# Kernel tuning notes

Hardware: AMD Instinct MI355X
Metric: run time of the kernel (lower is better)

## Reference

```python
import jax, jax.numpy as jnp
import numpy as np

K = 9  # knn kernel_size
SLOPE = 0.01  # LeakyReLU slope inside EdgeConv MLP (PyGraphBipartite default)


def setup_inputs() -> dict:
    key = jax.random.key(0)
    ks = jax.random.split(key, 5)
    B, C, H, W = 8, 96, 64, 64
    x = jax.random.normal(ks[0], (B, C, H, W), dtype=jnp.float32)
    # EdgeConv MLP: Linear(2C -> C), LeakyReLU(0.01), Linear(C -> C)
    W1 = jax.random.normal(ks[1], (2 * C, C), dtype=jnp.float32) * (1.0 / np.sqrt(2 * C))
    b1 = jax.random.normal(ks[2], (C,), dtype=jnp.float32) * 0.01
    W2 = jax.random.normal(ks[3], (C, C), dtype=jnp.float32) * (1.0 / np.sqrt(C))
    b2 = jax.random.normal(ks[4], (C,), dtype=jnp.float32) * 0.01
    return {"x": x, "W1": W1, "b1": b1, "W2": W2, "b2": b2}


def reference(x, W1, b1, W2, b2):
    B, C, H, W = x.shape
    M = H * W
    # flat_nodes: (B,C,H,W) -> per-image node features (B, M, C)
    xf = jnp.transpose(x, (0, 2, 3, 1)).reshape(B, M, C)

    # k-NN graph per image (batch-restricted), loop=True so self is a neighbor (dist 0)
    sq = jnp.sum(xf * xf, axis=-1)  # (B, M)
    dist = sq[:, :, None] + sq[:, None, :] - 2.0 * jnp.einsum("bmc,bnc->bmn", xf, xf)
    _, idx = jax.lax.top_k(-dist, K)  # (B, M, K) neighbor indices per center node

    # gather neighbor features: (B, M, K, C)
    xj = jax.vmap(lambda f, i: f[i])(xf, idx)
    xi = xf[:, :, None, :]  # center node, broadcast over K

    # EdgeConv message: MLP([x_i ; x_j - x_i]), then mean over neighbors
    feat = jnp.concatenate([jnp.broadcast_to(xi, xj.shape), xj - xi], axis=-1)  # (B,M,K,2C)
    h = feat @ W1 + b1
    h = jnp.where(h >= 0, h, SLOPE * h)  # LeakyReLU(0.01)
    h = h @ W2 + b2  # (B, M, K, C)
    out = jnp.mean(h, axis=2)  # mean aggregation -> (B, M, C)

    # norm='none' (Identity), act='relu'
    out = jax.nn.relu(out)

    # unflat_nodes: (B, M, C) -> (B, C, H, W)
    return jnp.transpose(out.reshape(B, H, W, C), (0, 3, 1, 2))
```

## Files before the change

kernel.cpp:

```cpp
#include <hip/hip_runtime.h>

#define B_ 8
#define C_ 96
#define CP_ 104
#define M_ 4096
#define K_ 9

typedef _Float16 f16x8 __attribute__((ext_vector_type(8)));
typedef float f32x4 __attribute__((ext_vector_type(4)));

typedef const __attribute__((address_space(1))) unsigned int* as1_u32p;
typedef __attribute__((address_space(3))) unsigned int* as3_u32p;

__device__ inline void g2lds16(const void* g, void* l) {
  __builtin_amdgcn_global_load_lds((as1_u32p)g, (as3_u32p)l, 16, 0, 0);
}

#define INSERT(dv, nv) do {                                                   \
    const int pz_ = tpos;                                                     \
    _Pragma("unroll")                                                         \
    for (int k_ = 0; k_ < K_; ++k_) if (k_ == pz_) { tv[k_] = (dv); ti[k_] = (nv); } \
    float mx_ = tv[0]; int mp_ = 0;                                           \
    _Pragma("unroll")                                                         \
    for (int k_ = 1; k_ < K_; ++k_) if (tv[k_] > mx_) { mx_ = tv[k_]; mp_ = k_; } \
    tmax = mx_; tpos = mp_;                                                   \
  } while (0)

__global__ __launch_bounds__(256) void prep1_kernel(
    const float* __restrict__ x, float* __restrict__ sq,
    unsigned short* __restrict__ xhi, unsigned short* __restrict__ xlo) {
  __shared__ float Xt[C_][64];
  const int b = blockIdx.y, m0 = blockIdx.x * 64, tid = threadIdx.x;
  const float* xb = x + (size_t)b * C_ * M_;
  for (int i = tid; i < C_ * 16; i += 256) {
    int c = i >> 4, j4 = (i & 15) << 2;
    *(float4*)&Xt[c][j4] = *(const float4*)&xb[(size_t)c * M_ + m0 + j4];
  }
  __syncthreads();
  if (tid < 64) {
    float s = 0.f;
#pragma unroll
    for (int c = 0; c < C_; ++c) { float v = Xt[c][tid]; s += v * v; }
    sq[b * M_ + m0 + tid] = s;
  }
  const int p = tid & 63, part = tid >> 6;
  union { unsigned short u[24]; uint4 q[3]; } hb, lb;
#pragma unroll
  for (int i = 0; i < 24; ++i) {
    float v = Xt[part * 24 + i][p];
    _Float16 h = (_Float16)v;
    _Float16 l = (_Float16)(v - (float)h);
    hb.u[i] = __builtin_bit_cast(unsigned short, h);
    lb.u[i] = __builtin_bit_cast(unsigned short, l);
  }
  size_t base = ((size_t)b * M_ + m0 + p) * CP_ + part * 24;
#pragma unroll
  for (int i = 0; i < 3; ++i) {
    *(uint4*)&xhi[base + i * 8] = hb.q[i];
    *(uint4*)&xlo[base + i * 8] = lb.q[i];
  }
}

__global__ __launch_bounds__(256, 3) void knn_kernel(
    const unsigned short* __restrict__ xhi, const unsigned short* __restrict__ xlo,
    const float* __restrict__ sq, int* __restrict__ idxw) {
  __shared__ struct { unsigned short bhi[64 * CP_]; unsigned short blo[64 * CP_]; } S[2];
  __shared__ float sqc[2][64];
  const int b = blockIdx.y, r0 = blockIdx.x * 64, tid = threadIdx.x;
  const int lane = tid & 63, w = tid >> 6;
  const int fp = lane & 15, kg = lane >> 4;
  const size_t bm = (size_t)b * M_;

  f16x8 qhi[3], qlo[3];
#pragma unroll
  for (int kt = 0; kt < 3; ++kt) {
    size_t off = (bm + r0 + w * 16 + fp) * CP_ + kt * 32 + kg * 8;
    qhi[kt] = *(const f16x8*)&xhi[off];
    qlo[kt] = *(const f16x8*)&xlo[off];
  }

  float tv[K_]; int ti[K_]; float tmax = 3.4e38f; int tpos = 0;
#pragma unroll
  for (int k = 0; k < K_; ++k) { tv[k] = 3.4e38f; ti[k] = 0; }

  auto stage = [&](int n0, int pp) {
    const unsigned short* sh = xhi + (bm + n0) * CP_;
    const unsigned short* sl = xlo + (bm + n0) * CP_;
    unsigned short* dh = S[pp].bhi;
    unsigned short* dl = S[pp].blo;
#pragma unroll
    for (int it = 0; it < 3; ++it) {
      int ch = tid + it * 256;
      g2lds16(sh + ch * 8, dh + ch * 8);
      g2lds16(sl + ch * 8, dl + ch * 8);
    }
    if (tid < 64) {
      int ch = 768 + tid;
      g2lds16(sh + ch * 8, dh + ch * 8);
      g2lds16(sl + ch * 8, dl + ch * 8);
      sqc[pp][tid] = sq[bm + n0 + tid];
    }
  };

  stage(0, 0);
  for (int t = 0; t < 64; ++t) {
    const int n0 = t * 64;
    const int cur = t & 1;
    __syncthreads();
    if (t < 63) stage(n0 + 64, cur ^ 1);

    float b0d = 0.f, b1d = 0.f; int b0n = 0, b1n = 0, bcnt = 0;

#pragma unroll
    for (int rs = 0; rs < 4; ++rs) {
      f16x8 nh[3], nl[3];
#pragma unroll
      for (int kt = 0; kt < 3; ++kt) {
        int boff = (rs * 16 + fp) * CP_ + kt * 32 + kg * 8;
        nh[kt] = *(const f16x8*)&S[cur].bhi[boff];
        nl[kt] = *(const f16x8*)&S[cur].blo[boff];
      }
      f32x4 acc = {0.f, 0.f, 0.f, 0.f};
#pragma unroll
      for (int kt = 0; kt < 3; ++kt) {
        acc = __builtin_amdgcn_mfma_f32_16x16x32_f16(nh[kt], qhi[kt], acc, 0, 0, 0);
        acc = __builtin_amdgcn_mfma_f32_16x16x32_f16(nh[kt], qlo[kt], acc, 0, 0, 0);
        acc = __builtin_amdgcn_mfma_f32_16x16x32_f16(nl[kt], qhi[kt], acc, 0, 0, 0);
      }
#pragma unroll
      for (int r = 0; r < 4; ++r) {
        const int nrow = rs * 16 + kg * 4 + r;
        const float d = sqc[cur][nrow] - 2.f * acc[r];
        if (d < tmax) {
          const int n = n0 + nrow;
          if (bcnt == 2) {
            if (b0d < tmax) INSERT(b0d, b0n);
            b0d = b1d; b0n = b1n;
            b1d = d;   b1n = n;
          } else if (bcnt == 1) {
            b1d = d; b1n = n; bcnt = 2;
          } else {
            b0d = d; b0n = n; bcnt = 1;
          }
        }
      }
    }
    if (bcnt >= 1 && b0d < tmax) INSERT(b0d, b0n);
    if (bcnt == 2 && b1d < tmax) INSERT(b1d, b1n);
  }

  __syncthreads();
  float* mv = (float*)&S[0];
  int*   mi = (int*)((char*)&S[0] + 64 * 37 * 4);
  const int qrow = w * 16 + fp;
#pragma unroll
  for (int k = 0; k < K_; ++k) {
    mv[qrow * 37 + kg * K_ + k] = tv[k];
    mi[qrow * 37 + kg * K_ + k] = ti[k];
  }
  __syncthreads();
  if (tid < 64) {
    float fv[K_]; int fi[K_];
    float mx = 3.4e38f; int mp = 0;
#pragma unroll
    for (int k = 0; k < K_; ++k) { fv[k] = 3.4e38f; fi[k] = 0; }
    for (int s = 0; s < 36; ++s) {
      float v = mv[tid * 37 + s]; int id = mi[tid * 37 + s];
      if (v < mx) {
#pragma unroll
        for (int k = 0; k < K_; ++k) if (k == mp) { fv[k] = v; fi[k] = id; }
        float m2 = fv[0]; int p2 = 0;
#pragma unroll
        for (int k = 1; k < K_; ++k) if (fv[k] > m2) { m2 = fv[k]; p2 = k; }
        mx = m2; mp = p2;
      }
    }
#pragma unroll
    for (int k = 0; k < K_; ++k)
      idxw[((size_t)b * M_ + r0 + tid) * K_ + k] = fi[k];
  }
}

__global__ __launch_bounds__(256) void prep2_kernel(
    const float* __restrict__ x, const float* __restrict__ W1,
    const float* __restrict__ b1, float* __restrict__ P, float* __restrict__ Q) {
  __shared__ float Xt[C_][64];
  __shared__ float Wt[C_][64];
  const int b = blockIdx.y, m0 = blockIdx.x * 64;
  const int tid = threadIdx.x;
  const float* xb = x + (size_t)b * C_ * M_;

  for (int i = tid; i < C_ * 16; i += 256) {
    int c = i >> 4, j4 = (i & 15) << 2;
    *(float4*)&Xt[c][j4] = *(const float4*)&xb[(size_t)c * M_ + m0 + j4];
  }

  const int ty = tid >> 4, tx = tid & 15;
  for (int t = 0; t < 3; ++t) {
    const int u0 = t * 64;
    __syncthreads();
    for (int i = tid; i < C_ * 64; i += 256) {
      int cin = i >> 6, j = i & 63;
      int u = u0 + j;
      float wv;
      if (u < C_) wv = W1[cin * C_ + u] - W1[(C_ + cin) * C_ + u];
      else        wv = W1[(C_ + cin) * C_ + (u - C_)];
      Wt[cin][j] = wv;
    }
    __syncthreads();
    float acc[4][4] = {};
#pragma unroll 8
    for (int c = 0; c < C_; ++c) {
      float4 rr = *(const float4*)&Xt[c][ty << 2];
      float4 ww = *(const float4*)&Wt[c][tx << 2];
      acc[0][0] += rr.x * ww.x; acc[0][1] += rr.x * ww.y; acc[0][2] += rr.x * ww.z; acc[0][3] += rr.x * ww.w;
      acc[1][0] += rr.y * ww.x; acc[1][1] += rr.y * ww.y; acc[1][2] += rr.y * ww.z; acc[1][3] += rr.y * ww.w;
      acc[2][0] += rr.z * ww.x; acc[2][1] += rr.z * ww.y; acc[2][2] += rr.z * ww.z; acc[2][3] += rr.z * ww.w;
      acc[3][0] += rr.w * ww.x; acc[3][1] += rr.w * ww.y; acc[3][2] += rr.w * ww.z; acc[3][3] += rr.w * ww.w;
    }
#pragma unroll
    for (int i = 0; i < 4; ++i) {
      int m = m0 + (ty << 2) + i;
      size_t base = ((size_t)b * M_ + m) * C_;
#pragma unroll
      for (int j = 0; j < 4; ++j) {
        int u = u0 + (tx << 2) + j;
        float v = acc[i][j];
        if (u < C_) P[base + u] = v + b1[u];
        else        Q[base + (u - C_)] = v;
      }
    }
  }
}

__global__ __launch_bounds__(256) void edge_mlp_kernel(
    const float* __restrict__ P, const float* __restrict__ Q,
    const int* __restrict__ idxw, const float* __restrict__ W2,
    const float* __restrict__ b2, float* __restrict__ out) {
  __shared__ float g_l[C_][64];
  __shared__ float W2t[C_ * C_];
  const int b = blockIdx.y, m0 = blockIdx.x * 64;
  const int tid = threadIdx.x;

  for (int i = tid; i < (C_ * C_) / 4; i += 256)
    *(float4*)&W2t[i * 4] = *(const float4*)&W2[i * 4];

  const int ml = tid & 63, cg = tid >> 6;
  const int m = m0 + ml;
  const float* prow = P + ((size_t)b * M_ + m) * C_ + cg * 24;
  float pr[24];
#pragma unroll
  for (int t = 0; t < 24; t += 4) {
    float4 v = *(const float4*)(prow + t);
    pr[t] = v.x; pr[t + 1] = v.y; pr[t + 2] = v.z; pr[t + 3] = v.w;
  }
  float gacc[24] = {};
  const int* irow = idxw + ((size_t)b * M_ + m) * K_;
#pragma unroll
  for (int k = 0; k < K_; ++k) {
    int j = irow[k];
    const float* qrow = Q + ((size_t)b * M_ + j) * C_ + cg * 24;
#pragma unroll
    for (int t = 0; t < 24; t += 4) {
      float4 qv = *(const float4*)(qrow + t);
      float h;
      h = pr[t + 0] + qv.x; gacc[t + 0] += (h >= 0.f) ? h : 0.01f * h;
      h = pr[t + 1] + qv.y; gacc[t + 1] += (h >= 0.f) ? h : 0.01f * h;
      h = pr[t + 2] + qv.z; gacc[t + 2] += (h >= 0.f) ? h : 0.01f * h;
      h = pr[t + 3] + qv.w; gacc[t + 3] += (h >= 0.f) ? h : 0.01f * h;
    }
  }
#pragma unroll
  for (int t = 0; t < 24; ++t) g_l[cg * 24 + t][ml] = gacc[t] * (1.f / 9.f);
  __syncthreads();

  const int ty = tid >> 4, tx = tid & 15;
  float acc2[4][6] = {};
#pragma unroll 4
  for (int c = 0; c < C_; ++c) {
    float4 rr = *(const float4*)&g_l[c][ty << 2];
    float2 wa = *(const float2*)&W2t[c * C_ + tx * 6];
    float2 wb = *(const float2*)&W2t[c * C_ + tx * 6 + 2];
    float2 wc = *(const float2*)&W2t[c * C_ + tx * 6 + 4];
    float rv[4] = {rr.x, rr.y, rr.z, rr.w};
    float wv[6] = {wa.x, wa.y, wb.x, wb.y, wc.x, wc.y};
#pragma unroll
    for (int i = 0; i < 4; ++i)
#pragma unroll
      for (int j = 0; j < 6; ++j) acc2[i][j] += rv[i] * wv[j];
  }
#pragma unroll
  for (int i = 0; i < 4; ++i) {
    int mm = m0 + (ty << 2) + i;
#pragma unroll
    for (int j = 0; j < 6; ++j) {
      int u = tx * 6 + j;
      float v = acc2[i][j] + b2[u];
      v = fmaxf(v, 0.f);
      out[((size_t)b * C_ + u) * M_ + mm] = v;
    }
  }
}

extern "C" void kernel_launch(void* const* d_in, const int* in_sizes, int n_in,
                              void* d_out, int out_size, void* d_ws, size_t ws_size,
                              hipStream_t stream) {
  const float* x  = (const float*)d_in[0];
  const float* W1 = (const float*)d_in[1];
  const float* b1 = (const float*)d_in[2];
  const float* W2 = (const float*)d_in[3];
  const float* b2 = (const float*)d_in[4];
  float* out = (float*)d_out;

  char* ws = (char*)d_ws;
  float* sq  = (float*)ws;
  int* idxw  = (int*)(ws + 131072);
  unsigned short* xhi = (unsigned short*)(ws + 1310720);
  unsigned short* xlo = (unsigned short*)(ws + 8126464);
  float* P = (float*)(ws + 1310720);
  float* Q = (float*)(ws + 13893632);

  dim3 grid(M_ / 64, B_), blk(256);
  prep1_kernel<<<grid, blk, 0, stream>>>(x, sq, xhi, xlo);
  knn_kernel<<<grid, blk, 0, stream>>>(xhi, xlo, sq, idxw);
  prep2_kernel<<<grid, blk, 0, stream>>>(x, W1, b1, P, Q);
  edge_mlp_kernel<<<grid, blk, 0, stream>>>(P, Q, idxw, W2, b2, out);
}
```

Before: 297.2 us.

## Split kNN candidate range across blocks, read neighbors directly from global, add merge kernel

The kNN kernel now splits each query tile's candidate range into two halves handled by separate blocks (grid z dimension), which doubles the number of blocks to improve occupancy and load balance. Each half writes its partial top-9 distances and indices to workspace, and a new merge kernel combines them. The LDS double-buffered staging through global_load_lds is removed in favour of direct per-lane global loads of neighbor fragments, relying on L2/L1 hits, and launch bounds are raised to 4 blocks per CU. Costs include an extra kernel launch, extra workspace traffic, and losing explicit LDS reuse of neighbor tiles across the four waves.

```diff
diff --git a/kernel.cpp b/kernel.cpp
--- a/kernel.cpp
+++ b/kernel.cpp
@@ -5,16 +5,11 @@
 #define CP_ 104
 #define M_ 4096
 #define K_ 9
+#define NSPLIT 2
+#define NHALF (M_ / NSPLIT)
 
 typedef _Float16 f16x8 __attribute__((ext_vector_type(8)));
 typedef float f32x4 __attribute__((ext_vector_type(4)));
-
-typedef const __attribute__((address_space(1))) unsigned int* as1_u32p;
-typedef __attribute__((address_space(3))) unsigned int* as3_u32p;
-
-__device__ inline void g2lds16(const void* g, void* l) {
-  __builtin_amdgcn_global_load_lds((as1_u32p)g, (as3_u32p)l, 16, 0, 0);
-}
 
 #define INSERT(dv, nv) do {                                                   \
     const int pz_ = tpos;                                                     \
@@ -61,15 +56,17 @@
   }
 }
 
-__global__ __launch_bounds__(256, 3) void knn_kernel(
+__global__ __launch_bounds__(256, 4) void knn_kernel(
     const unsigned short* __restrict__ xhi, const unsigned short* __restrict__ xlo,
-    const float* __restrict__ sq, int* __restrict__ idxw) {
-  __shared__ struct { unsigned short bhi[64 * CP_]; unsigned short blo[64 * CP_]; } S[2];
-  __shared__ float sqc[2][64];
-  const int b = blockIdx.y, r0 = blockIdx.x * 64, tid = threadIdx.x;
+    const float* __restrict__ sq, float* __restrict__ pv, int* __restrict__ pi) {
+  __shared__ float mv[64 * 37];
+  __shared__ int   mi[64 * 37];
+  const int b = blockIdx.y, r0 = blockIdx.x * 64, h = blockIdx.z;
+  const int tid = threadIdx.x;
   const int lane = tid & 63, w = tid >> 6;
   const int fp = lane & 15, kg = lane >> 4;
   const size_t bm = (size_t)b * M_;
+  const int nbeg = h * NHALF;
 
   f16x8 qhi[3], qlo[3];
 #pragma unroll
@@ -83,56 +80,38 @@
 #pragma unroll
   for (int k = 0; k < K_; ++k) { tv[k] = 3.4e38f; ti[k] = 0; }
 
-  auto stage = [&](int n0, int pp) {
-    const unsigned short* sh = xhi + (bm + n0) * CP_;
-    const unsigned short* sl = xlo + (bm + n0) * CP_;
-    unsigned short* dh = S[pp].bhi;
-    unsigned short* dl = S[pp].blo;
-#pragma unroll
-    for (int it = 0; it < 3; ++it) {
-      int ch = tid + it * 256;
-      g2lds16(sh + ch * 8, dh + ch * 8);
-      g2lds16(sl + ch * 8, dl + ch * 8);
-    }
-    if (tid < 64) {
-      int ch = 768 + tid;
-      g2lds16(sh + ch * 8, dh + ch * 8);
-      g2lds16(sl + ch * 8, dl + ch * 8);
-      sqc[pp][tid] = sq[bm + n0 + tid];
-    }
-  };
-
-  stage(0, 0);
-  for (int t = 0; t < 64; ++t) {
-    const int n0 = t * 64;
-    const int cur = t & 1;
-    __syncthreads();
-    if (t < 63) stage(n0 + 64, cur ^ 1);
-
+  const unsigned short* nbh = xhi + (bm + nbeg + fp) * CP_ + kg * 8;
+  const unsigned short* nbl = xlo + (bm + nbeg + fp) * CP_ + kg * 8;
+  const float* sqb = sq + bm + nbeg + kg * 4;
+
+  for (int t = 0; t < NHALF / 64; ++t) {
+    const int tb = t * 64;
     float b0d = 0.f, b1d = 0.f; int b0n = 0, b1n = 0, bcnt = 0;
-
 #pragma unroll
     for (int rs = 0; rs < 4; ++rs) {
-      f16x8 nh[3], nl[3];
-#pragma unroll
-      for (int kt = 0; kt < 3; ++kt) {
-        int boff = (rs * 16 + fp) * CP_ + kt * 32 + kg * 8;
-        nh[kt] = *(const f16x8*)&S[cur].bhi[boff];
-        nl[kt] = *(const f16x8*)&S[cur].blo[boff];
-      }
+      const size_t ro = (size_t)(tb + rs * 16) * CP_;
+      f16x8 nh0 = *(const f16x8*)(nbh + ro);
+      f16x8 nh1 = *(const f16x8*)(nbh + ro + 32);
+      f16x8 nh2 = *(const f16x8*)(nbh + ro + 64);
+      f16x8 nl0 = *(const f16x8*)(nbl + ro);
+      f16x8 nl1 = *(const f16x8*)(nbl + ro + 32);
+      f16x8 nl2 = *(const f16x8*)(nbl + ro + 64);
+      const f32x4 sqv = *(const f32x4*)&sqb[tb + rs * 16];
       f32x4 acc = {0.f, 0.f, 0.f, 0.f};
-#pragma unroll
-      for (int kt = 0; kt < 3; ++kt) {
-        acc = __builtin_amdgcn_mfma_f32_16x16x32_f16(nh[kt], qhi[kt], acc, 0, 0, 0);
-        acc = __builtin_amdgcn_mfma_f32_16x16x32_f16(nh[kt], qlo[kt], acc, 0, 0, 0);
-        acc = __builtin_amdgcn_mfma_f32_16x16x32_f16(nl[kt], qhi[kt], acc, 0, 0, 0);
-      }
+      acc = __builtin_amdgcn_mfma_f32_16x16x32_f16(nh0, qhi[0], acc, 0, 0, 0);
+      acc = __builtin_amdgcn_mfma_f32_16x16x32_f16(nh1, qhi[1], acc, 0, 0, 0);
+      acc = __builtin_amdgcn_mfma_f32_16x16x32_f16(nh2, qhi[2], acc, 0, 0, 0);
+      acc = __builtin_amdgcn_mfma_f32_16x16x32_f16(nh0, qlo[0], acc, 0, 0, 0);
+      acc = __builtin_amdgcn_mfma_f32_16x16x32_f16(nh1, qlo[1], acc, 0, 0, 0);
+      acc = __builtin_amdgcn_mfma_f32_16x16x32_f16(nh2, qlo[2], acc, 0, 0, 0);
+      acc = __builtin_amdgcn_mfma_f32_16x16x32_f16(nl0, qhi[0], acc, 0, 0, 0);
+      acc = __builtin_amdgcn_mfma_f32_16x16x32_f16(nl1, qhi[1], acc, 0, 0, 0);
+      acc = __builtin_amdgcn_mfma_f32_16x16x32_f16(nl2, qhi[2], acc, 0, 0, 0);
 #pragma unroll
       for (int r = 0; r < 4; ++r) {
-        const int nrow = rs * 16 + kg * 4 + r;
-        const float d = sqc[cur][nrow] - 2.f * acc[r];
+        const float d = sqv[r] - 2.f * acc[r];
         if (d < tmax) {
-          const int n = n0 + nrow;
+          const int n = nbeg + tb + rs * 16 + kg * 4 + r;
           if (bcnt == 2) {
             if (b0d < tmax) INSERT(b0d, b0n);
             b0d = b1d; b0n = b1n;
@@ -149,9 +128,6 @@
     if (bcnt == 2 && b1d < tmax) INSERT(b1d, b1n);
   }
 
-  __syncthreads();
-  float* mv = (float*)&S[0];
-  int*   mi = (int*)((char*)&S[0] + 64 * 37 * 4);
   const int qrow = w * 16 + fp;
 #pragma unroll
   for (int k = 0; k < K_; ++k) {
@@ -175,10 +151,35 @@
         mx = m2; mp = p2;
       }
     }
-#pragma unroll
-    for (int k = 0; k < K_; ++k)
-      idxw[((size_t)b * M_ + r0 + tid) * K_ + k] = fi[k];
-  }
+    size_t base = ((size_t)h * B_ * M_ + bm + r0 + tid) * K_;
+#pragma unroll
+    for (int k = 0; k < K_; ++k) { pv[base + k] = fv[k]; pi[base + k] = fi[k]; }
+  }
+}
+
+__global__ __launch_bounds__(256) void knn_merge_kernel(
+    const float* __restrict__ pv, const int* __restrict__ pi,
+    int* __restrict__ idxw) {
+  const int g = blockIdx.x * 256 + threadIdx.x;
+  float tv[K_]; int ti[K_]; float tmax = 3.4e38f; int tpos = 0;
+#pragma unroll
+  for (int k = 0; k < K_; ++k) { tv[k] = 3.4e38f; ti[k] = 0; }
+  const float* v0 = pv + (size_t)g * K_;
+  const int*   i0 = pi + (size_t)g * K_;
+  const float* v1 = pv + ((size_t)B_ * M_ + g) * K_;
+  const int*   i1 = pi + ((size_t)B_ * M_ + g) * K_;
+#pragma unroll
+  for (int s = 0; s < K_; ++s) {
+    float d = v0[s];
+    if (d < tmax) { int n = i0[s]; INSERT(d, n); }
+  }
+#pragma unroll
+  for (int s = 0; s < K_; ++s) {
+    float d = v1[s];
+    if (d < tmax) { int n = i1[s]; INSERT(d, n); }
+  }
+#pragma unroll
+  for (int k = 0; k < K_; ++k) idxw[(size_t)g * K_ + k] = ti[k];
 }
 
 __global__ __launch_bounds__(256) void prep2_kernel(
@@ -317,12 +318,15 @@
   int* idxw  = (int*)(ws + 131072);
   unsigned short* xhi = (unsigned short*)(ws + 1310720);
   unsigned short* xlo = (unsigned short*)(ws + 8126464);
+  float* pv = (float*)(ws + 14942208);
+  int*   pi = (int*)(ws + 17301504);
   float* P = (float*)(ws + 1310720);
   float* Q = (float*)(ws + 13893632);
 
-  dim3 grid(M_ / 64, B_), blk(256);
-  prep1_kernel<<<grid, blk, 0, stream>>>(x, sq, xhi, xlo);
-  knn_kernel<<<grid, blk, 0, stream>>>(xhi, xlo, sq, idxw);
-  prep2_kernel<<<grid, blk, 0, stream>>>(x, W1, b1, P, Q);
-  edge_mlp_kernel<<<grid, blk, 0, stream>>>(P, Q, idxw, W2, b2, out);
-}
+  dim3 blk(256);
+  prep1_kernel<<<dim3(M_ / 64, B_), blk, 0, stream>>>(x, sq, xhi, xlo);
+  knn_kernel<<<dim3(M_ / 64, B_, NSPLIT), blk, 0, stream>>>(xhi, xlo, sq, pv, pi);
+  knn_merge_kernel<<<dim3(B_ * M_ / 256), blk, 0, stream>>>(pv, pi, idxw);
+  prep2_kernel<<<dim3(M_ / 64, B_), blk, 0, stream>>>(x, W1, b1, P, Q);
+  edge_mlp_kernel<<<dim3(M_ / 64, B_), blk, 0, stream>>>(P, Q, idxw, W2, b2, out);
+}
```

Measured after the change: 313.1 us. +5.3%, slower.

## Split kNN candidate scan across blocks and merge partial top-k lists

Applied to the files above, without the earlier changes.

Adds a third grid dimension that splits each query tile's scan over candidate nodes into four independent chunks. Each chunk writes its partial top-9 distances and indices to workspace, and a new merge kernel combines them into the final index list. The aim is to raise block count and waves per CU so the MFMA-based distance scan hides latency better, at the cost of an extra launch and extra global traffic for the partial results. The two-entry candidate buffer is also now flushed only once after the tile loop, instead of after every tile.

```diff
diff --git a/kernel.cpp b/kernel.cpp
--- a/kernel.cpp
+++ b/kernel.cpp
@@ -5,6 +5,9 @@
 #define CP_ 104
 #define M_ 4096
 #define K_ 9
+#define NSPLIT 4
+#define NPART (M_ / NSPLIT)
+#define NTILES (NPART / 64)
 
 typedef _Float16 f16x8 __attribute__((ext_vector_type(8)));
 typedef float f32x4 __attribute__((ext_vector_type(4)));
@@ -63,13 +66,15 @@
 
 __global__ __launch_bounds__(256, 3) void knn_kernel(
     const unsigned short* __restrict__ xhi, const unsigned short* __restrict__ xlo,
-    const float* __restrict__ sq, int* __restrict__ idxw) {
+    const float* __restrict__ sq, float* __restrict__ pv, int* __restrict__ pi) {
   __shared__ struct { unsigned short bhi[64 * CP_]; unsigned short blo[64 * CP_]; } S[2];
   __shared__ float sqc[2][64];
-  const int b = blockIdx.y, r0 = blockIdx.x * 64, tid = threadIdx.x;
+  const int b = blockIdx.y, r0 = blockIdx.x * 64, h = blockIdx.z;
+  const int tid = threadIdx.x;
   const int lane = tid & 63, w = tid >> 6;
   const int fp = lane & 15, kg = lane >> 4;
   const size_t bm = (size_t)b * M_;
+  const int nbeg = h * NPART;
 
   f16x8 qhi[3], qlo[3];
 #pragma unroll
@@ -102,14 +107,14 @@
     }
   };
 
-  stage(0, 0);
-  for (int t = 0; t < 64; ++t) {
-    const int n0 = t * 64;
+  float b0d = 0.f, b1d = 0.f; int b0n = 0, b1n = 0, bcnt = 0;
+
+  stage(nbeg, 0);
+  for (int t = 0; t < NTILES; ++t) {
+    const int n0 = nbeg + t * 64;
     const int cur = t & 1;
     __syncthreads();
-    if (t < 63) stage(n0 + 64, cur ^ 1);
-
-    float b0d = 0.f, b1d = 0.f; int b0n = 0, b1n = 0, bcnt = 0;
+    if (t < NTILES - 1) stage(n0 + 64, cur ^ 1);
 
 #pragma unroll
     for (int rs = 0; rs < 4; ++rs) {
@@ -145,9 +150,9 @@
         }
       }
     }
-    if (bcnt >= 1 && b0d < tmax) INSERT(b0d, b0n);
-    if (bcnt == 2 && b1d < tmax) INSERT(b1d, b1n);
-  }
+  }
+  if (bcnt >= 1 && b0d < tmax) INSERT(b0d, b0n);
+  if (bcnt == 2 && b1d < tmax) INSERT(b1d, b1n);
 
   __syncthreads();
   float* mv = (float*)&S[0];
@@ -175,10 +180,31 @@
         mx = m2; mp = p2;
       }
     }
-#pragma unroll
-    for (int k = 0; k < K_; ++k)
-      idxw[((size_t)b * M_ + r0 + tid) * K_ + k] = fi[k];
-  }
+    size_t base = ((size_t)h * B_ * M_ + bm + r0 + tid) * K_;
+#pragma unroll
+    for (int k = 0; k < K_; ++k) { pv[base + k] = fv[k]; pi[base + k] = fi[k]; }
+  }
+}
+
+__global__ __launch_bounds__(256) void knn_merge_kernel(
+    const float* __restrict__ pv, const int* __restrict__ pi,
+    int* __restrict__ idxw) {
+  const int g = blockIdx.x * 256 + threadIdx.x;
+  float tv[K_]; int ti[K_]; float tmax = 3.4e38f; int tpos = 0;
+#pragma unroll
+  for (int k = 0; k < K_; ++k) { tv[k] = 3.4e38f; ti[k] = 0; }
+#pragma unroll
+  for (int h = 0; h < NSPLIT; ++h) {
+    const float* vs = pv + ((size_t)h * B_ * M_ + g) * K_;
+    const int*   is = pi + ((size_t)h * B_ * M_ + g) * K_;
+#pragma unroll
+    for (int s = 0; s < K_; ++s) {
+      float d = vs[s];
+      if (d < tmax) { int n = is[s]; INSERT(d, n); }
+    }
+  }
+#pragma unroll
+  for (int k = 0; k < K_; ++k) idxw[(size_t)g * K_ + k] = ti[k];
 }
 
 __global__ __launch_bounds__(256) void prep2_kernel(
@@ -317,12 +343,15 @@
   int* idxw  = (int*)(ws + 131072);
   unsigned short* xhi = (unsigned short*)(ws + 1310720);
   unsigned short* xlo = (unsigned short*)(ws + 8126464);
+  float* pv = (float*)(ws + 14942208);
+  int*   pi = (int*)(ws + 19660800);
   float* P = (float*)(ws + 1310720);
   float* Q = (float*)(ws + 13893632);
 
-  dim3 grid(M_ / 64, B_), blk(256);
-  prep1_kernel<<<grid, blk, 0, stream>>>(x, sq, xhi, xlo);
-  knn_kernel<<<grid, blk, 0, stream>>>(xhi, xlo, sq, idxw);
-  prep2_kernel<<<grid, blk, 0, stream>>>(x, W1, b1, P, Q);
-  edge_mlp_kernel<<<grid, blk, 0, stream>>>(P, Q, idxw, W2, b2, out);
-}
+  dim3 blk(256);
+  prep1_kernel<<<dim3(M_ / 64, B_), blk, 0, stream>>>(x, sq, xhi, xlo);
+  knn_kernel<<<dim3(M_ / 64, B_, NSPLIT), blk, 0, stream>>>(xhi, xlo, sq, pv, pi);
+  knn_merge_kernel<<<dim3(B_ * M_ / 256), blk, 0, stream>>>(pv, pi, idxw);
+  prep2_kernel<<<dim3(M_ / 64, B_), blk, 0, stream>>>(x, W1, b1, P, Q);
+  edge_mlp_kernel<<<dim3(M_ / 64, B_), blk, 0, stream>>>(P, Q, idxw, W2, b2, out);
+}
```

After: 469.1 us. 1.58x slower.
